# Optimization experiments

Hardware: AMD Instinct MI355X
Metric: run time of the kernel (lower is better)

Reference implementation:

```python
import jax, jax.numpy as jnp
import numpy as np

B, N, IN_F, OUT_F, H = 16, 1024, 256, 256, 4
D = OUT_F // H  # head_dim = 64
NEG_SLOPE = 0.2


def setup_inputs() -> dict:
    key = jax.random.key(0)
    k1, k2, k3 = jax.random.split(key, 3)
    h = jax.random.normal(k1, (B, N, IN_F), dtype=jnp.float32)
    mask = jnp.ones((B, N), dtype=jnp.int32)
    W = jax.random.normal(k2, (OUT_F, IN_F), dtype=jnp.float32) * (1.0 / np.sqrt(IN_F))
    a = jax.random.normal(k3, (2 * D, 1), dtype=jnp.float32) * 0.1
    return {"h": h, "mask": mask, "W": W, "a": a}


def reference(h, mask, W, a):
    # Wh = h @ W.T -> (B, N, OUT_F) -> (B, H, N, D)
    Wh = jnp.einsum('bnf,of->bno', h, W)
    Wh = Wh.reshape(h.shape[0], h.shape[1], H, D).transpose(0, 2, 1, 3)
    # Additive split: cat([Wh_i, Wh_j]) @ a == Wh_i @ a1 + Wh_j @ a2 (same math,
    # avoids the O(N^2 * 2D) concat tensor)
    a1 = a[:D, 0]  # (D,)
    a2 = a[D:, 0]  # (D,)
    s1 = jnp.einsum('bhnd,d->bhn', Wh, a1)  # score for node i
    s2 = jnp.einsum('bhnd,d->bhn', Wh, a2)  # score for node j
    e = s1[:, :, :, None] + s2[:, :, None, :]          # (B, H, N, N)
    e = jnp.where(e >= 0, e, NEG_SLOPE * e)            # LeakyReLU(0.2)
    node_mask = mask.astype(bool)                      # (B, N)
    mm = node_mask[:, None, :, None] & node_mask[:, None, None, :]  # (B,1,N,N)
    e = jnp.where(mm, e, -jnp.inf)
    attn = jax.nn.softmax(e, axis=-1)
    # dropout is identity in eval mode
    attn = jnp.where(mm, attn, 0.0)
    h_prime = jnp.einsum('bhij,bhjd->bhid', attn, Wh)  # (B, H, N, D)
    h_prime = h_prime.transpose(0, 2, 1, 3).reshape(h.shape[0], h.shape[1], OUT_F)
    return h_prime * mask.astype(h_prime.dtype)[:, :, None]
```

## Files before the change

kernel.cpp:

```cpp
#include <hip/hip_runtime.h>

typedef short short8 __attribute__((ext_vector_type(8)));
typedef float floatx4 __attribute__((ext_vector_type(4)));
typedef float floatx16 __attribute__((ext_vector_type(16)));
typedef unsigned int u32;

#define NEG_SLOPE 0.2f

__device__ __forceinline__ u32 pk_rtne(float a, float b) {
    u32 ua = __float_as_uint(a); ua += 0x7fffu + ((ua >> 16) & 1u);
    u32 ub = __float_as_uint(b); ub += 0x7fffu + ((ub >> 16) & 1u);
    return __builtin_amdgcn_perm(ub, ua, 0x07060302);
}
__device__ __forceinline__ u32 pk_trunc(float a, float b) {
    return __builtin_amdgcn_perm(__float_as_uint(b), __float_as_uint(a), 0x07060302);
}
__device__ __forceinline__ void gl_lds16(const void* g, void* l) {
    __builtin_amdgcn_global_load_lds((__attribute__((address_space(1))) u32*)(void*)g,
                                     (__attribute__((address_space(3))) u32*)l, 16, 0, 0);
}

__global__ __launch_bounds__(256, 4) void k_wh(
    const float* __restrict__ hin, const int* __restrict__ mask,
    const float* __restrict__ W, const float* __restrict__ a,
    unsigned short* __restrict__ WhF, float2* __restrict__ E1F1,
    float2* __restrict__ E2F2)
{
    __shared__ unsigned short sBF[8 * 4 * 64 * 8];
    __shared__ float sV1[256], sV2[256];

    const int t = threadIdx.x;
    const int bi = blockIdx.x;
    const int mtile = bi & 255, hh = bi >> 8;
    const int m0g = mtile * 64;
    const int b = m0g >> 10, i0 = m0g & 1023;
    const int b4h = b * 4 + hh;
    const int wid = t >> 6, lane = t & 63;
    const int l15 = lane & 15, q = lane >> 4;

    sV1[t] = 0.f;
    sV2[t] = 0.f;
    __syncthreads();

    float vp1[8] = {0, 0, 0, 0, 0, 0, 0, 0};
    float vp2[8] = {0, 0, 0, 0, 0, 0, 0, 0};
    {
        const int c = t & 31;
        const int rb = t >> 5;
#pragma unroll
        for (int i = 0; i < 8; ++i) {
            int row = i * 8 + rb;
            const float* gp = &W[((size_t)(hh * 64 + row)) * 256 + c * 8];
            float4 w0 = *(const float4*)gp;
            float4 w1 = *(const float4*)(gp + 4);
            float a1r = a[row], a2r = a[64 + row];
            vp1[0] += a1r * w0.x; vp1[1] += a1r * w0.y; vp1[2] += a1r * w0.z; vp1[3] += a1r * w0.w;
            vp1[4] += a1r * w1.x; vp1[5] += a1r * w1.y; vp1[6] += a1r * w1.z; vp1[7] += a1r * w1.w;
            vp2[0] += a2r * w0.x; vp2[1] += a2r * w0.y; vp2[2] += a2r * w0.z; vp2[3] += a2r * w0.w;
            vp2[4] += a2r * w1.x; vp2[5] += a2r * w1.y; vp2[6] += a2r * w1.z; vp2[7] += a2r * w1.w;
            uint4 pv;
            pv.x = pk_rtne(w0.x, w0.y); pv.y = pk_rtne(w0.z, w0.w);
            pv.z = pk_rtne(w1.x, w1.y); pv.w = pk_rtne(w1.z, w1.w);
            int kt = c >> 2, qq = c & 3, nt = row >> 4, r15 = row & 15;
            int idx16 = (kt * 4 + nt) * 64 + qq * 16 + r15;
            *(uint4*)&sBF[(idx16 ^ kt) * 8] = pv;
        }
    }
#pragma unroll
    for (int j = 0; j < 8; ++j) {
        vp1[j] += __shfl_xor(vp1[j], 32, 64);
        vp2[j] += __shfl_xor(vp2[j], 32, 64);
    }
    if (lane < 32) {
        const int c = t & 31;
#pragma unroll
        for (int j = 0; j < 8; ++j) {
            atomicAdd(&sV1[c * 8 + j], vp1[j]);
            atomicAdd(&sV2[c * 8 + j], vp2[j]);
        }
    }
    __syncthreads();

    floatx4 acc[4];
#pragma unroll
    for (int nt = 0; nt < 4; ++nt) {
        floatx4 z = {0.f, 0.f, 0.f, 0.f};
        acc[nt] = z;
    }
    float s1a = 0.f, s2a = 0.f;
    const float* hrow = &hin[((size_t)(m0g + wid * 16 + l15)) * 256 + q * 8];
#pragma unroll
    for (int kt = 0; kt < 8; ++kt) {
        float4 h0 = *(const float4*)(hrow + kt * 32);
        float4 h1 = *(const float4*)(hrow + kt * 32 + 4);
        float4 v1a = *(const float4*)&sV1[kt * 32 + q * 8];
        float4 v1b = *(const float4*)&sV1[kt * 32 + q * 8 + 4];
        float4 v2a = *(const float4*)&sV2[kt * 32 + q * 8];
        float4 v2b = *(const float4*)&sV2[kt * 32 + q * 8 + 4];
        s1a += h0.x * v1a.x + h0.y * v1a.y + h0.z * v1a.z + h0.w * v1a.w
             + h1.x * v1b.x + h1.y * v1b.y + h1.z * v1b.z + h1.w * v1b.w;
        s2a += h0.x * v2a.x + h0.y * v2a.y + h0.z * v2a.z + h0.w * v2a.w
             + h1.x * v2b.x + h1.y * v2b.y + h1.z * v2b.z + h1.w * v2b.w;
        union { short8 s; uint4 u; } af;
        af.u.x = pk_rtne(h0.x, h0.y); af.u.y = pk_rtne(h0.z, h0.w);
        af.u.z = pk_rtne(h1.x, h1.y); af.u.w = pk_rtne(h1.z, h1.w);
#pragma unroll
        for (int nt = 0; nt < 4; ++nt) {
            int idx16 = (kt * 4 + nt) * 64 + lane;
            short8 bf = *(const short8*)&sBF[(idx16 ^ kt) * 8];
            acc[nt] = __builtin_amdgcn_mfma_f32_16x16x32_bf16(af.s, bf, acc[nt], 0, 0, 0);
        }
    }

    const int jt16 = (i0 >> 4) + wid;
    const int g = q & 1, jb = (q >> 1) * 4;
#pragma unroll
    for (int nt = 0; nt < 4; ++nt) {
        int nt32 = nt >> 1;
        int l31 = (nt & 1) * 16 + l15;
        uint2 pv;
        pv.x = pk_rtne(acc[nt][0], acc[nt][1]);
        pv.y = pk_rtne(acc[nt][2], acc[nt][3]);
        size_t idx = ((((size_t)b4h * 64 + jt16) * 2 + nt32) * 64 + (g * 32 + l31)) * 8 + jb;
        *(uint2*)&WhF[idx] = pv;
    }

    s1a += __shfl_xor(s1a, 16, 64); s1a += __shfl_xor(s1a, 32, 64);
    s2a += __shfl_xor(s2a, 16, 64); s2a += __shfl_xor(s2a, 32, 64);
    if (lane < 16) {
        int i = i0 + wid * 16 + lane;
        E1F1[(size_t)b4h * 1024 + i] = make_float2(__expf(s1a), __expf(NEG_SLOPE * s1a));
        int mj = mask[b * 1024 + i];
        E2F2[(size_t)b4h * 1024 + i] =
            make_float2(mj ? __expf(s2a) : 0.f, mj ? __expf(NEG_SLOPE * s2a) : 0.f);
    }
}

__global__ __launch_bounds__(256, 2) void k_attn(
    const int* __restrict__ mask,
    const unsigned short* __restrict__ WhF,
    const float2* __restrict__ E1F1, const float2* __restrict__ E2F2,
    float* __restrict__ out)
{
    __shared__ unsigned short sB[2][8192];
    __shared__ float2 sEF[2][128];

    const int t = threadIdx.x;
    const int bi = blockIdx.x;
    const int b4h = bi & 63, ib = bi >> 6;
    const int b = b4h >> 2, hh = b4h & 3;
    const int i0 = ib * 128;
    const int wid = t >> 6, lane = t & 63;
    const int l31 = lane & 31, g = lane >> 5;
    const int iw = i0 + wid * 32;

    float2 e1 = E1F1[(size_t)b4h * 1024 + iw + l31];
    const float E1 = e1.x, F1 = e1.y;

    floatx16 acc0, acc1, accL;
#pragma unroll
    for (int r = 0; r < 16; ++r) { acc0[r] = 0.f; acc1[r] = 0.f; accL[r] = 0.f; }
    const short ob = (short)0x3F80;
    const short8 ones = {ob, ob, ob, ob, ob, ob, ob, ob};

    const char* gbase = (const char*)WhF + (size_t)b4h * 131072;

    {
#pragma unroll
        for (int i = 0; i < 4; ++i)
            gl_lds16(gbase + wid * 4096 + i * 1024 + lane * 16,
                     (char*)&sB[0][0] + wid * 4096 + i * 1024);
        if (wid == 1)
            gl_lds16((const char*)&E2F2[(size_t)b4h * 1024] + lane * 16, (char*)&sEF[0][0]);
    }

    for (int jt = 0; jt < 8; ++jt) {
        const int buf = jt & 1;
        __syncthreads();
        if (jt < 7) {
            const char* gp = gbase + (size_t)(jt + 1) * 16384;
#pragma unroll
            for (int i = 0; i < 4; ++i)
                gl_lds16(gp + wid * 4096 + i * 1024 + lane * 16,
                         (char*)&sB[buf ^ 1][0] + wid * 4096 + i * 1024);
            if (wid == 1)
                gl_lds16((const char*)&E2F2[(size_t)b4h * 1024 + (jt + 1) * 128] + lane * 16,
                         (char*)&sEF[buf ^ 1][0]);
        }
#pragma unroll
        for (int tl = 0; tl < 8; ++tl) {
            const float4 eA0 = *(const float4*)&sEF[buf][tl * 16 + g * 4];
            const float4 eA1 = *(const float4*)&sEF[buf][tl * 16 + g * 4 + 2];
            const float4 eB0 = *(const float4*)&sEF[buf][tl * 16 + 8 + g * 4];
            const float4 eB1 = *(const float4*)&sEF[buf][tl * 16 + 8 + g * 4 + 2];
            float w0 = fmaxf(E1 * eA0.x, F1 * eA0.y);
            float w1 = fmaxf(E1 * eA0.z, F1 * eA0.w);
            float w2 = fmaxf(E1 * eA1.x, F1 * eA1.y);
            float w3 = fmaxf(E1 * eA1.z, F1 * eA1.w);
            float w4 = fmaxf(E1 * eB0.x, F1 * eB0.y);
            float w5 = fmaxf(E1 * eB0.z, F1 * eB0.w);
            float w6 = fmaxf(E1 * eB1.x, F1 * eB1.y);
            float w7 = fmaxf(E1 * eB1.z, F1 * eB1.w);
            union { short8 s; u32 u[4]; } af;
            af.u[0] = pk_trunc(w0, w1);
            af.u[1] = pk_trunc(w2, w3);
            af.u[2] = pk_trunc(w4, w5);
            af.u[3] = pk_trunc(w6, w7);
            short8 bf0 = *(const short8*)&sB[buf][((tl * 2 + 0) * 64 + lane) * 8];
            short8 bf1 = *(const short8*)&sB[buf][((tl * 2 + 1) * 64 + lane) * 8];
            acc0 = __builtin_amdgcn_mfma_f32_32x32x16_bf16(af.s, bf0, acc0, 0, 0, 0);
            acc1 = __builtin_amdgcn_mfma_f32_32x32x16_bf16(af.s, bf1, acc1, 0, 0, 0);
            accL = __builtin_amdgcn_mfma_f32_32x32x16_bf16(af.s, ones, accL, 0, 0, 0);
        }
    }

#pragma unroll
    for (int r = 0; r < 16; ++r) {
        int row = (r & 3) + 8 * (r >> 2) + 4 * g;
        int i = iw + row;
        float l = accL[r];
        int mi = mask[b * 1024 + i];
        float inv = (mi && l > 0.f) ? 1.0f / l : 0.f;
        size_t o = ((size_t)(b * 1024 + i)) * 256 + hh * 64;
        out[o + l31] = acc0[r] * inv;
        out[o + 32 + l31] = acc1[r] * inv;
    }
}

extern "C" void kernel_launch(void* const* d_in, const int* in_sizes, int n_in,
                              void* d_out, int out_size, void* d_ws, size_t ws_size,
                              hipStream_t stream) {
    const float* h = (const float*)d_in[0];
    const int* mask = (const int*)d_in[1];
    const float* W = (const float*)d_in[2];
    const float* a = (const float*)d_in[3];
    float* out = (float*)d_out;

    unsigned short* WhF = (unsigned short*)d_ws;
    float2* E1F1 = (float2*)((char*)d_ws + (size_t)64 * 64 * 2 * 64 * 8 * 2);
    float2* E2F2 = E1F1 + 64 * 1024;

    hipLaunchKernelGGL(k_wh, dim3(1024), dim3(256), 0, stream, h, mask, W, a, WhF, E1F1, E2F2);
    hipLaunchKernelGGL(k_attn, dim3(512), dim3(256), 0, stream, mask, WhF, E1F1, E2F2, out);
}
```

Baseline: 104.3 us.

## Drop per-row exp factor and split j-range across wave pairs sharing B fragments

The LeakyReLU-softmax weight max(E1*E2, F1*F2) is rescaled per row by 1/E1, so only one factor G1=exp(-0.8*s1) is stored and applied. This is exact because softmax normalisation cancels per-row scaling. Each wave now computes 64 rows over half of each 128-column j tile, so every B fragment and edge-score load from LDS feeds two row groups. The two halves are then summed through an LDS scratch reduction. This cuts the VALU multiplies and LDS reads per MFMA, at the cost of more accumulator registers (six 16-wide accumulators instead of three) and extra barriers and LDS traffic in the epilogue.

```diff
diff --git a/kernel.cpp b/kernel.cpp
--- a/kernel.cpp
+++ b/kernel.cpp
@@ -23,7 +23,7 @@
 __global__ __launch_bounds__(256, 4) void k_wh(
     const float* __restrict__ hin, const int* __restrict__ mask,
     const float* __restrict__ W, const float* __restrict__ a,
-    unsigned short* __restrict__ WhF, float2* __restrict__ E1F1,
+    unsigned short* __restrict__ WhF, float* __restrict__ G1,
     float2* __restrict__ E2F2)
 {
     __shared__ unsigned short sBF[8 * 4 * 64 * 8];
@@ -129,7 +129,7 @@
     s2a += __shfl_xor(s2a, 16, 64); s2a += __shfl_xor(s2a, 32, 64);
     if (lane < 16) {
         int i = i0 + wid * 16 + lane;
-        E1F1[(size_t)b4h * 1024 + i] = make_float2(__expf(s1a), __expf(NEG_SLOPE * s1a));
+        G1[(size_t)b4h * 1024 + i] = __expf(-0.8f * s1a);
         int mj = mask[b * 1024 + i];
         E2F2[(size_t)b4h * 1024 + i] =
             make_float2(mj ? __expf(s2a) : 0.f, mj ? __expf(NEG_SLOPE * s2a) : 0.f);
@@ -139,7 +139,7 @@
 __global__ __launch_bounds__(256, 2) void k_attn(
     const int* __restrict__ mask,
     const unsigned short* __restrict__ WhF,
-    const float2* __restrict__ E1F1, const float2* __restrict__ E2F2,
+    const float* __restrict__ G1, const float2* __restrict__ E2F2,
     float* __restrict__ out)
 {
     __shared__ unsigned short sB[2][8192];
@@ -152,14 +152,18 @@
     const int i0 = ib * 128;
     const int wid = t >> 6, lane = t & 63;
     const int l31 = lane & 31, g = lane >> 5;
-    const int iw = i0 + wid * 32;
-
-    float2 e1 = E1F1[(size_t)b4h * 1024 + iw + l31];
-    const float E1 = e1.x, F1 = e1.y;
-
-    floatx16 acc0, acc1, accL;
-#pragma unroll
-    for (int r = 0; r < 16; ++r) { acc0[r] = 0.f; acc1[r] = 0.f; accL[r] = 0.f; }
+    const int pair = wid >> 1, half = wid & 1;
+    const int iw = i0 + pair * 64;
+
+    const float g1a = G1[(size_t)b4h * 1024 + iw + l31];
+    const float g1b = G1[(size_t)b4h * 1024 + iw + 32 + l31];
+
+    floatx16 acc00, acc01, acc10, acc11, accL0, accL1;
+#pragma unroll
+    for (int r = 0; r < 16; ++r) {
+        acc00[r] = 0.f; acc01[r] = 0.f; acc10[r] = 0.f;
+        acc11[r] = 0.f; accL0[r] = 0.f; accL1[r] = 0.f;
+    }
     const short ob = (short)0x3F80;
     const short8 ones = {ob, ob, ob, ob, ob, ob, ob, ob};
 
@@ -188,42 +192,83 @@
                          (char*)&sEF[buf ^ 1][0]);
         }
 #pragma unroll
-        for (int tl = 0; tl < 8; ++tl) {
-            const float4 eA0 = *(const float4*)&sEF[buf][tl * 16 + g * 4];
-            const float4 eA1 = *(const float4*)&sEF[buf][tl * 16 + g * 4 + 2];
-            const float4 eB0 = *(const float4*)&sEF[buf][tl * 16 + 8 + g * 4];
-            const float4 eB1 = *(const float4*)&sEF[buf][tl * 16 + 8 + g * 4 + 2];
-            float w0 = fmaxf(E1 * eA0.x, F1 * eA0.y);
-            float w1 = fmaxf(E1 * eA0.z, F1 * eA0.w);
-            float w2 = fmaxf(E1 * eA1.x, F1 * eA1.y);
-            float w3 = fmaxf(E1 * eA1.z, F1 * eA1.w);
-            float w4 = fmaxf(E1 * eB0.x, F1 * eB0.y);
-            float w5 = fmaxf(E1 * eB0.z, F1 * eB0.w);
-            float w6 = fmaxf(E1 * eB1.x, F1 * eB1.y);
-            float w7 = fmaxf(E1 * eB1.z, F1 * eB1.w);
-            union { short8 s; u32 u[4]; } af;
-            af.u[0] = pk_trunc(w0, w1);
-            af.u[1] = pk_trunc(w2, w3);
-            af.u[2] = pk_trunc(w4, w5);
-            af.u[3] = pk_trunc(w6, w7);
+        for (int tl4 = 0; tl4 < 4; ++tl4) {
+            const int tl = half * 4 + tl4;
+            const int jb = tl * 16;
+            const float4 eA0 = *(const float4*)&sEF[buf][jb + g * 4];
+            const float4 eA1 = *(const float4*)&sEF[buf][jb + g * 4 + 2];
+            const float4 eB0 = *(const float4*)&sEF[buf][jb + 8 + g * 4];
+            const float4 eB1 = *(const float4*)&sEF[buf][jb + 8 + g * 4 + 2];
+            union { short8 s; u32 u[4]; } af0, af1;
+            af0.u[0] = pk_trunc(fmaxf(eA0.x, g1a * eA0.y), fmaxf(eA0.z, g1a * eA0.w));
+            af0.u[1] = pk_trunc(fmaxf(eA1.x, g1a * eA1.y), fmaxf(eA1.z, g1a * eA1.w));
+            af0.u[2] = pk_trunc(fmaxf(eB0.x, g1a * eB0.y), fmaxf(eB0.z, g1a * eB0.w));
+            af0.u[3] = pk_trunc(fmaxf(eB1.x, g1a * eB1.y), fmaxf(eB1.z, g1a * eB1.w));
+            af1.u[0] = pk_trunc(fmaxf(eA0.x, g1b * eA0.y), fmaxf(eA0.z, g1b * eA0.w));
+            af1.u[1] = pk_trunc(fmaxf(eA1.x, g1b * eA1.y), fmaxf(eA1.z, g1b * eA1.w));
+            af1.u[2] = pk_trunc(fmaxf(eB0.x, g1b * eB0.y), fmaxf(eB0.z, g1b * eB0.w));
+            af1.u[3] = pk_trunc(fmaxf(eB1.x, g1b * eB1.y), fmaxf(eB1.z, g1b * eB1.w));
             short8 bf0 = *(const short8*)&sB[buf][((tl * 2 + 0) * 64 + lane) * 8];
             short8 bf1 = *(const short8*)&sB[buf][((tl * 2 + 1) * 64 + lane) * 8];
-            acc0 = __builtin_amdgcn_mfma_f32_32x32x16_bf16(af.s, bf0, acc0, 0, 0, 0);
-            acc1 = __builtin_amdgcn_mfma_f32_32x32x16_bf16(af.s, bf1, acc1, 0, 0, 0);
-            accL = __builtin_amdgcn_mfma_f32_32x32x16_bf16(af.s, ones, accL, 0, 0, 0);
+            acc00 = __builtin_amdgcn_mfma_f32_32x32x16_bf16(af0.s, bf0, acc00, 0, 0, 0);
+            acc01 = __builtin_amdgcn_mfma_f32_32x32x16_bf16(af0.s, bf1, acc01, 0, 0, 0);
+            acc10 = __builtin_amdgcn_mfma_f32_32x32x16_bf16(af1.s, bf0, acc10, 0, 0, 0);
+            acc11 = __builtin_amdgcn_mfma_f32_32x32x16_bf16(af1.s, bf1, acc11, 0, 0, 0);
+            accL0 = __builtin_amdgcn_mfma_f32_32x32x16_bf16(af0.s, ones, accL0, 0, 0, 0);
+            accL1 = __builtin_amdgcn_mfma_f32_32x32x16_bf16(af1.s, ones, accL1, 0, 0, 0);
+        }
+    }
+
+    __syncthreads();
+    {
+        float* sScr = (float*)&sB[0][0];
+        const int base = pair * 3072 + lane;
+        if (half == 1) {
+#pragma unroll
+            for (int r = 0; r < 16; ++r) {
+                sScr[base + r * 64]        = acc00[r];
+                sScr[base + (r + 16) * 64] = acc01[r];
+                sScr[base + (r + 32) * 64] = accL0[r];
+            }
+        }
+        __syncthreads();
+        if (half == 0) {
+#pragma unroll
+            for (int r = 0; r < 16; ++r) {
+                acc00[r] += sScr[base + r * 64];
+                acc01[r] += sScr[base + (r + 16) * 64];
+                accL0[r] += sScr[base + (r + 32) * 64];
+            }
+#pragma unroll
+            for (int r = 0; r < 16; ++r) {
+                sScr[base + r * 64]        = acc10[r];
+                sScr[base + (r + 16) * 64] = acc11[r];
+                sScr[base + (r + 32) * 64] = accL1[r];
+            }
+        }
+        __syncthreads();
+        if (half == 1) {
+#pragma unroll
+            for (int r = 0; r < 16; ++r) {
+                acc10[r] += sScr[base + r * 64];
+                acc11[r] += sScr[base + (r + 16) * 64];
+                accL1[r] += sScr[base + (r + 32) * 64];
+            }
         }
     }
 
 #pragma unroll
     for (int r = 0; r < 16; ++r) {
         int row = (r & 3) + 8 * (r >> 2) + 4 * g;
-        int i = iw + row;
-        float l = accL[r];
+        int i = iw + half * 32 + row;
+        float aA = half ? acc10[r] : acc00[r];
+        float aB = half ? acc11[r] : acc01[r];
+        float l  = half ? accL1[r] : accL0[r];
         int mi = mask[b * 1024 + i];
         float inv = (mi && l > 0.f) ? 1.0f / l : 0.f;
         size_t o = ((size_t)(b * 1024 + i)) * 256 + hh * 64;
-        out[o + l31] = acc0[r] * inv;
-        out[o + 32 + l31] = acc1[r] * inv;
+        out[o + l31] = aA * inv;
+        out[o + 32 + l31] = aB * inv;
     }
 }
 
@@ -237,9 +282,9 @@
     float* out = (float*)d_out;
 
     unsigned short* WhF = (unsigned short*)d_ws;
-    float2* E1F1 = (float2*)((char*)d_ws + (size_t)64 * 64 * 2 * 64 * 8 * 2);
-    float2* E2F2 = E1F1 + 64 * 1024;
-
-    hipLaunchKernelGGL(k_wh, dim3(1024), dim3(256), 0, stream, h, mask, W, a, WhF, E1F1, E2F2);
-    hipLaunchKernelGGL(k_attn, dim3(512), dim3(256), 0, stream, mask, WhF, E1F1, E2F2, out);
-}
+    float* G1 = (float*)((char*)d_ws + (size_t)64 * 64 * 2 * 64 * 8 * 2);
+    float2* E2F2 = (float2*)(G1 + 64 * 1024);
+
+    hipLaunchKernelGGL(k_wh, dim3(1024), dim3(256), 0, stream, h, mask, W, a, WhF, G1, E2F2);
+    hipLaunchKernelGGL(k_attn, dim3(512), dim3(256), 0, stream, mask, WhF, G1, E2F2, out);
+}
```

Result: no change. 104.4 us (+0.1%).
